# Kernel optimization log

Hardware: AMD Instinct MI355X
Metric: run time of the kernel (lower is better)

The kernel has to match this reference:

```python
import jax, jax.numpy as jnp
import numpy as np

N_NODES = 200000
D_IN = 256
D_OUT = 256
B = 4096
K1 = 25   # layer-1 fanout
K2 = 10   # layer-2 fanout
M = B * (1 + K2)  # layer-1 node set size: batch centers + their sampled neighbors


def setup_inputs() -> dict:
    key = jax.random.key(0)
    k1, k2, k3, k4, k5, k6 = jax.random.split(key, 6)
    features = jax.random.normal(k1, (N_NODES, D_IN), dtype=jnp.float32)
    # SageLayer weights: [out, 2*in] (concat path, gcn=False); small kaiming-like scale
    W1 = jax.random.normal(k2, (D_OUT, 2 * D_IN), dtype=jnp.float32) * 0.05
    W2 = jax.random.normal(k3, (D_OUT, 2 * D_OUT), dtype=jnp.float32) * 0.05
    nodes_batch = jax.random.randint(k4, (B,), 0, N_NODES, dtype=jnp.int64)
    neigh2 = jax.random.randint(k5, (B, K2), 0, N_NODES, dtype=jnp.int64)
    neigh1 = jax.random.randint(k6, (M, K1), 0, N_NODES, dtype=jnp.int64)
    return {"features": features, "W1": W1, "W2": W2,
            "nodes_batch": nodes_batch, "neigh2": neigh2, "neigh1": neigh1}


def reference(features, W1, W2, nodes_batch, neigh2, neigh1):
    # Layer-1 node set: centers first, then their sampled layer-2 neighbors.
    l1_nodes = jnp.concatenate([nodes_batch, neigh2.reshape(-1)])  # [M]
    # ---- layer 1: MEAN aggregate over K1 sampled neighbors (gather + mean) ----
    agg1 = jnp.mean(features[neigh1], axis=1)          # [M, K1, D_IN] -> [M, D_IN]
    self1 = features[l1_nodes]                         # [M, D_IN]
    # SageLayer: relu(W.mm(cat(self, agg).T)).T == relu(cat @ W.T)
    h1 = jax.nn.relu(jnp.concatenate([self1, agg1], axis=1) @ W1.T)  # [M, D_OUT]
    # ---- layer 2: centers are h1[:B]; neighbor embeddings are h1[B:] in blocks of K2 ----
    nb = nodes_batch.shape[0]
    agg2 = jnp.mean(h1[nb:].reshape(nb, -1, h1.shape[1]), axis=1)    # [B, D_OUT]
    h2 = jax.nn.relu(jnp.concatenate([h1[:nb], agg2], axis=1) @ W2.T)  # [B, D_OUT]
    return h2
```

## Files before the change

kernel.cpp:

```cpp
#include <hip/hip_runtime.h>
#include <hip/hip_bf16.h>

typedef __attribute__((ext_vector_type(8))) short bf16x8;
typedef __attribute__((ext_vector_type(4))) float f32x4;
typedef __attribute__((ext_vector_type(2))) float f32x2;

#define B_SZ   4096
#define K1     25
#define K2     10
#define M_L1   45056
#define D      256
#define K_DIM  512
#define N_NODES 200000

static __device__ __forceinline__ unsigned short f2bf(float f) {
    union { float f; unsigned u; } v; v.f = f;
    return (unsigned short)((v.u + 0x7fffu + ((v.u >> 16) & 1u)) >> 16);
}
static __device__ __forceinline__ float bf2f(unsigned short h) {
    union { unsigned u; float f; } v; v.u = ((unsigned)h) << 16;
    return v.f;
}

__global__ __launch_bounds__(256)
void convert_fp8(const float* __restrict__ f, unsigned* __restrict__ f8) {
    const size_t i = ((size_t)blockIdx.x * 256 + threadIdx.x) * 8;
    const float4 a = *(const float4*)(f + i);
    const float4 b = *(const float4*)(f + i + 4);
    unsigned u0 = 0, u1 = 0;
    u0 = __builtin_amdgcn_cvt_pk_fp8_f32(a.x, a.y, u0, false);
    u0 = __builtin_amdgcn_cvt_pk_fp8_f32(a.z, a.w, u0, true);
    u1 = __builtin_amdgcn_cvt_pk_fp8_f32(b.x, b.y, u1, false);
    u1 = __builtin_amdgcn_cvt_pk_fp8_f32(b.z, b.w, u1, true);
    uint2 r; r.x = u0; r.y = u1;
    *(uint2*)(f8 + (i >> 2)) = r;
}

__global__ __launch_bounds__(256)
void convert_w(const float* __restrict__ W1, const float* __restrict__ W2,
               unsigned short* __restrict__ W1b, unsigned short* __restrict__ W2b) {
    const int i = blockIdx.x * 256 + threadIdx.x;
    W1b[i] = f2bf(W1[i]);
    W2b[i] = f2bf(W2[i]);
}

__global__ __launch_bounds__(256)
void agg1_kernel(const float* __restrict__ feat,
                 const unsigned* __restrict__ f8,
                 const int* __restrict__ nodes_batch,
                 const int* __restrict__ neigh2,
                 const int* __restrict__ neigh1,
                 unsigned short* __restrict__ X1) {
    const int wave = threadIdx.x >> 6;
    const int lane = threadIdx.x & 63;
    const int m = (blockIdx.x << 2) + wave;
    const int self_node = (m < B_SZ) ? nodes_batch[m] : neigh2[m - B_SZ];
    const int* nb = neigh1 + (size_t)m * K1;

    int idxv = (lane < K1) ? nb[lane] : 0;
    const float4 s = *(const float4*)(feat + (size_t)self_node * D + (lane << 2));

    unsigned q[K1];
    #pragma unroll
    for (int j = 0; j < K1; ++j) {
        const int node = __shfl(idxv, j);
        q[j] = f8[(size_t)node * (D / 4) + lane];
    }

    float a0 = 0.f, a1 = 0.f, a2 = 0.f, a3 = 0.f;
    #pragma unroll
    for (int j = 0; j < K1; ++j) {
        const f32x2 lo = __builtin_amdgcn_cvt_pk_f32_fp8(q[j], false);
        const f32x2 hi = __builtin_amdgcn_cvt_pk_f32_fp8(q[j], true);
        a0 += lo.x; a1 += lo.y; a2 += hi.x; a3 += hi.y;
    }
    const float inv = 1.0f / (float)K1;

    unsigned short* xr = X1 + (size_t)m * K_DIM;
    *(ushort4*)(xr + (lane << 2)) =
        make_ushort4(f2bf(s.x), f2bf(s.y), f2bf(s.z), f2bf(s.w));
    *(ushort4*)(xr + D + (lane << 2)) =
        make_ushort4(f2bf(a0 * inv), f2bf(a1 * inv), f2bf(a2 * inv), f2bf(a3 * inv));
}

__global__ __launch_bounds__(256)
void agg2_kernel(const unsigned short* __restrict__ h1,
                 unsigned short* __restrict__ X2) {
    const int wave = threadIdx.x >> 6;
    const int lane = threadIdx.x & 63;
    const int b = (blockIdx.x << 2) + wave;
    const ushort4 s = *(const ushort4*)(h1 + (size_t)b * D + (lane << 2));
    float sx = 0.f, sy = 0.f, sz = 0.f, sw = 0.f;
    #pragma unroll
    for (int k = 0; k < K2; ++k) {
        const ushort4 v = *(const ushort4*)(h1 + (size_t)(B_SZ + b * K2 + k) * D + (lane << 2));
        sx += bf2f(v.x); sy += bf2f(v.y); sz += bf2f(v.z); sw += bf2f(v.w);
    }
    const float inv = 1.0f / (float)K2;
    unsigned short* xr = X2 + (size_t)b * K_DIM;
    *(ushort4*)(xr + (lane << 2)) = s;
    *(ushort4*)(xr + D + (lane << 2)) =
        make_ushort4(f2bf(sx * inv), f2bf(sy * inv), f2bf(sz * inv), f2bf(sw * inv));
}

template<bool OUT_BF16>
__global__ __launch_bounds__(256)
void gemm_relu(const unsigned short* __restrict__ A,
               const unsigned short* __restrict__ W,
               void* __restrict__ Cout) {
    __shared__ unsigned short As[128 * 64];
    __shared__ unsigned short Bs[128 * 64];
    const int tid  = threadIdx.x;
    const int w    = tid >> 6, lane = tid & 63;
    const int quad = lane >> 4, l16 = lane & 15;
    const int wm = (w >> 1) << 6;
    const int wn = (w & 1) << 6;
    const size_t row0 = (size_t)blockIdx.x * 128;
    const size_t col0 = (size_t)blockIdx.y * 128;

    const int srow   = (w << 5) + (lane >> 3);
    const int schunk = ((lane & 7) ^ (lane >> 3)) << 3;
    const unsigned short* aG = A + (row0 + srow) * K_DIM + schunk;
    const unsigned short* bG = W + (col0 + srow) * K_DIM + schunk;

    f32x4 acc[4][4];
    #pragma unroll
    for (int i = 0; i < 4; ++i)
        #pragma unroll
        for (int j = 0; j < 4; ++j)
            acc[i][j] = (f32x4){0.f, 0.f, 0.f, 0.f};

    for (int k0 = 0; k0 < K_DIM; k0 += 64) {
        __syncthreads();
        #pragma unroll
        for (int n = 0; n < 4; ++n) {
            __builtin_amdgcn_global_load_lds(
                (const __attribute__((address_space(1))) void*)(aG + (size_t)(n * 8) * K_DIM + k0),
                (__attribute__((address_space(3))) void*)(As + ((w << 2) + n) * 512),
                16, 0, 0);
            __builtin_amdgcn_global_load_lds(
                (const __attribute__((address_space(1))) void*)(bG + (size_t)(n * 8) * K_DIM + k0),
                (__attribute__((address_space(3))) void*)(Bs + ((w << 2) + n) * 512),
                16, 0, 0);
        }
        __syncthreads();
        #pragma unroll
        for (int ks = 0; ks < 2; ++ks) {
            bf16x8 af[4], bfr[4];
            #pragma unroll
            for (int i = 0; i < 4; ++i) {
                const int row = wm + i * 16 + l16;
                af[i] = *(const bf16x8*)&As[row * 64 + ((((ks << 2) + quad) ^ (l16 & 7)) << 3)];
            }
            #pragma unroll
            for (int i = 0; i < 4; ++i) {
                const int row = wn + i * 16 + l16;
                bfr[i] = *(const bf16x8*)&Bs[row * 64 + ((((ks << 2) + quad) ^ (l16 & 7)) << 3)];
            }
            #pragma unroll
            for (int mi = 0; mi < 4; ++mi)
                #pragma unroll
                for (int ni = 0; ni < 4; ++ni)
                    acc[mi][ni] = __builtin_amdgcn_mfma_f32_16x16x32_bf16(
                        af[mi], bfr[ni], acc[mi][ni], 0, 0, 0);
        }
    }

    #pragma unroll
    for (int mi = 0; mi < 4; ++mi) {
        #pragma unroll
        for (int ni = 0; ni < 4; ++ni) {
            #pragma unroll
            for (int r = 0; r < 4; ++r) {
                const size_t gm = row0 + wm + mi * 16 + quad * 4 + r;
                const size_t gn = col0 + wn + ni * 16 + l16;
                float v = acc[mi][ni][r];
                v = v > 0.f ? v : 0.f;
                if (OUT_BF16)
                    ((unsigned short*)Cout)[gm * D + gn] = f2bf(v);
                else
                    ((float*)Cout)[gm * D + gn] = v;
            }
        }
    }
}

extern "C" void kernel_launch(void* const* d_in, const int* in_sizes, int n_in,
                              void* d_out, int out_size, void* d_ws, size_t ws_size,
                              hipStream_t stream) {
    const float* feat        = (const float*)d_in[0];
    const float* W1          = (const float*)d_in[1];
    const float* W2          = (const float*)d_in[2];
    const int*   nodes_batch = (const int*)d_in[3];
    const int*   neigh2      = (const int*)d_in[4];
    const int*   neigh1      = (const int*)d_in[5];
    float* out = (float*)d_out;

    char* ws = (char*)d_ws;
    unsigned*       f8   = (unsigned*)(ws);
    unsigned short* X1   = (unsigned short*)(ws + 51200000);
    unsigned short* h1   = (unsigned short*)(ws + 51200000 + 46137344);
    unsigned short* X2   = (unsigned short*)(ws + 51200000 + 46137344 + 23068672);
    unsigned short* W1b  = (unsigned short*)(ws + 51200000 + 46137344 + 23068672 + 4194304);
    unsigned short* W2b  = (unsigned short*)(ws + 51200000 + 46137344 + 23068672 + 4194304 + 262144);

    convert_fp8<<<25000, 256, 0, stream>>>(feat, f8);
    convert_w<<<512, 256, 0, stream>>>(W1, W2, W1b, W2b);
    agg1_kernel<<<M_L1 / 4, 256, 0, stream>>>(feat, f8, nodes_batch, neigh2, neigh1, X1);
    gemm_relu<true><<<dim3(M_L1 / 128, 2), 256, 0, stream>>>(X1, W1b, h1);
    agg2_kernel<<<B_SZ / 4, 256, 0, stream>>>(h1, X2);
    gemm_relu<false><<<dim3(B_SZ / 128, 2), 256, 0, stream>>>(X2, W2b, out);
}
```

Before: 378.1 us.

## Double-buffer GEMM K-loop, full-width N tiles, and fuse weight conversion

```diff
diff --git a/kernel.cpp b/kernel.cpp
--- a/kernel.cpp
+++ b/kernel.cpp
@@ -13,6 +13,9 @@
 #define K_DIM  512
 #define N_NODES 200000
 
+#define AS1 __attribute__((address_space(1)))
+#define AS3 __attribute__((address_space(3)))
+
 static __device__ __forceinline__ unsigned short f2bf(float f) {
     union { float f; unsigned u; } v; v.f = f;
     return (unsigned short)((v.u + 0x7fffu + ((v.u >> 16) & 1u)) >> 16);
@@ -23,7 +26,9 @@
 }
 
 __global__ __launch_bounds__(256)
-void convert_fp8(const float* __restrict__ f, unsigned* __restrict__ f8) {
+void convert_all(const float* __restrict__ f, unsigned* __restrict__ f8,
+                 const float* __restrict__ W1, const float* __restrict__ W2,
+                 unsigned short* __restrict__ W1b, unsigned short* __restrict__ W2b) {
     const size_t i = ((size_t)blockIdx.x * 256 + threadIdx.x) * 8;
     const float4 a = *(const float4*)(f + i);
     const float4 b = *(const float4*)(f + i + 4);
@@ -34,14 +39,11 @@
     u1 = __builtin_amdgcn_cvt_pk_fp8_f32(b.z, b.w, u1, true);
     uint2 r; r.x = u0; r.y = u1;
     *(uint2*)(f8 + (i >> 2)) = r;
-}
-
-__global__ __launch_bounds__(256)
-void convert_w(const float* __restrict__ W1, const float* __restrict__ W2,
-               unsigned short* __restrict__ W1b, unsigned short* __restrict__ W2b) {
-    const int i = blockIdx.x * 256 + threadIdx.x;
-    W1b[i] = f2bf(W1[i]);
-    W2b[i] = f2bf(W2[i]);
+    const int j = blockIdx.x * 256 + threadIdx.x;
+    if (j < D * K_DIM) {
+        W1b[j] = f2bf(W1[j]);
+        W2b[j] = f2bf(W2[j]);
+    }
 }
 
 __global__ __launch_bounds__(256)
@@ -103,77 +105,89 @@
         make_ushort4(f2bf(sx * inv), f2bf(sy * inv), f2bf(sz * inv), f2bf(sw * inv));
 }
 
-template<bool OUT_BF16>
+template<int BM, bool OUT_BF16>
 __global__ __launch_bounds__(256)
 void gemm_relu(const unsigned short* __restrict__ A,
                const unsigned short* __restrict__ W,
                void* __restrict__ Cout) {
-    __shared__ unsigned short As[128 * 64];
-    __shared__ unsigned short Bs[128 * 64];
+    constexpr int MFR = BM / 16;
+    constexpr int ACALLS = BM / 8;
+    __shared__ unsigned short As[2][BM * 64];
+    __shared__ unsigned short Bs[2][256 * 64];
     const int tid  = threadIdx.x;
     const int w    = tid >> 6, lane = tid & 63;
     const int quad = lane >> 4, l16 = lane & 15;
-    const int wm = (w >> 1) << 6;
-    const int wn = (w & 1) << 6;
-    const size_t row0 = (size_t)blockIdx.x * 128;
-    const size_t col0 = (size_t)blockIdx.y * 128;
-
-    const int srow   = (w << 5) + (lane >> 3);
-    const int schunk = ((lane & 7) ^ (lane >> 3)) << 3;
+    const int wn   = w << 6;
+    const size_t row0 = (size_t)blockIdx.x * BM;
+
+    const int srow   = lane >> 3;
+    const int schunk = ((lane & 7) ^ srow) << 3;
     const unsigned short* aG = A + (row0 + srow) * K_DIM + schunk;
-    const unsigned short* bG = W + (col0 + srow) * K_DIM + schunk;
-
-    f32x4 acc[4][4];
-    #pragma unroll
-    for (int i = 0; i < 4; ++i)
+    const unsigned short* bG = W + (size_t)srow * K_DIM + schunk;
+
+    f32x4 acc[MFR][4];
+    #pragma unroll
+    for (int i = 0; i < MFR; ++i)
         #pragma unroll
         for (int j = 0; j < 4; ++j)
             acc[i][j] = (f32x4){0.f, 0.f, 0.f, 0.f};
 
-    for (int k0 = 0; k0 < K_DIM; k0 += 64) {
-        __syncthreads();
-        #pragma unroll
-        for (int n = 0; n < 4; ++n) {
+    auto stage = [&](int buf, int k0) {
+        #pragma unroll
+        for (int c = w; c < ACALLS; c += 4)
             __builtin_amdgcn_global_load_lds(
-                (const __attribute__((address_space(1))) void*)(aG + (size_t)(n * 8) * K_DIM + k0),
-                (__attribute__((address_space(3))) void*)(As + ((w << 2) + n) * 512),
-                16, 0, 0);
+                (const AS1 void*)(aG + (size_t)(c * 8) * K_DIM + k0),
+                (AS3 void*)(&As[buf][c * 512]), 16, 0, 0);
+        #pragma unroll
+        for (int c = w; c < 32; c += 4)
             __builtin_amdgcn_global_load_lds(
-                (const __attribute__((address_space(1))) void*)(bG + (size_t)(n * 8) * K_DIM + k0),
-                (__attribute__((address_space(3))) void*)(Bs + ((w << 2) + n) * 512),
-                16, 0, 0);
-        }
-        __syncthreads();
+                (const AS1 void*)(bG + (size_t)(c * 8) * K_DIM + k0),
+                (AS3 void*)(&Bs[buf][c * 512]), 16, 0, 0);
+    };
+
+    auto compute = [&](int buf) {
         #pragma unroll
         for (int ks = 0; ks < 2; ++ks) {
-            bf16x8 af[4], bfr[4];
-            #pragma unroll
-            for (int i = 0; i < 4; ++i) {
-                const int row = wm + i * 16 + l16;
-                af[i] = *(const bf16x8*)&As[row * 64 + ((((ks << 2) + quad) ^ (l16 & 7)) << 3)];
+            bf16x8 af[MFR], bfr[4];
+            #pragma unroll
+            for (int i = 0; i < MFR; ++i) {
+                const int row = i * 16 + l16;
+                af[i] = *(const bf16x8*)&As[buf][row * 64 + ((((ks << 2) + quad) ^ (l16 & 7)) << 3)];
             }
             #pragma unroll
             for (int i = 0; i < 4; ++i) {
                 const int row = wn + i * 16 + l16;
-                bfr[i] = *(const bf16x8*)&Bs[row * 64 + ((((ks << 2) + quad) ^ (l16 & 7)) << 3)];
+                bfr[i] = *(const bf16x8*)&Bs[buf][row * 64 + ((((ks << 2) + quad) ^ (l16 & 7)) << 3)];
             }
             #pragma unroll
-            for (int mi = 0; mi < 4; ++mi)
+            for (int mi = 0; mi < MFR; ++mi)
                 #pragma unroll
                 for (int ni = 0; ni < 4; ++ni)
                     acc[mi][ni] = __builtin_amdgcn_mfma_f32_16x16x32_bf16(
                         af[mi], bfr[ni], acc[mi][ni], 0, 0, 0);
         }
-    }
-
-    #pragma unroll
-    for (int mi = 0; mi < 4; ++mi) {
+    };
+
+    stage(0, 0);
+    asm volatile("s_waitcnt vmcnt(0)" ::: "memory");
+    __syncthreads();
+    #pragma unroll
+    for (int t = 0; t < 7; ++t) {
+        stage((t & 1) ^ 1, (t + 1) << 6);
+        compute(t & 1);
+        asm volatile("s_waitcnt vmcnt(0)" ::: "memory");
+        __syncthreads();
+    }
+    compute(1);
+
+    #pragma unroll
+    for (int mi = 0; mi < MFR; ++mi) {
         #pragma unroll
         for (int ni = 0; ni < 4; ++ni) {
             #pragma unroll
             for (int r = 0; r < 4; ++r) {
-                const size_t gm = row0 + wm + mi * 16 + quad * 4 + r;
-                const size_t gn = col0 + wn + ni * 16 + l16;
+                const size_t gm = row0 + mi * 16 + quad * 4 + r;
+                const size_t gn = (size_t)wn + ni * 16 + l16;
                 float v = acc[mi][ni][r];
                 v = v > 0.f ? v : 0.f;
                 if (OUT_BF16)
@@ -204,10 +218,9 @@
     unsigned short* W1b  = (unsigned short*)(ws + 51200000 + 46137344 + 23068672 + 4194304);
     unsigned short* W2b  = (unsigned short*)(ws + 51200000 + 46137344 + 23068672 + 4194304 + 262144);
 
-    convert_fp8<<<25000, 256, 0, stream>>>(feat, f8);
-    convert_w<<<512, 256, 0, stream>>>(W1, W2, W1b, W2b);
+    convert_all<<<25000, 256, 0, stream>>>(feat, f8, W1, W2, W1b, W2b);
     agg1_kernel<<<M_L1 / 4, 256, 0, stream>>>(feat, f8, nodes_batch, neigh2, neigh1, X1);
-    gemm_relu<true><<<dim3(M_L1 / 128, 2), 256, 0, stream>>>(X1, W1b, h1);
+    gemm_relu<64, true><<<M_L1 / 64, 256, 0, stream>>>(X1, W1b, h1);
     agg2_kernel<<<B_SZ / 4, 256, 0, stream>>>(h1, X2);
-    gemm_relu<false><<<dim3(B_SZ / 128, 2), 256, 0, stream>>>(X2, W2b, out);
-}
+    gemm_relu<16, false><<<B_SZ / 16, 256, 0, stream>>>(X2, W2b, out);
+}
```

After: 383.5 us. About the same (+1.4%).
